# Kernel tuning notes

Hardware: AMD Instinct MI355X
Metric: run time of the kernel (lower is better)

## Reference

```python
import jax, jax.numpy as jnp
import numpy as np

B = 32768
STATE_DIM = 64
ACTION_DIM = 16
HIDDEN = 512
ENSEMBLE = 7
TOP_K = 5
IN_DIM = STATE_DIM + ACTION_DIM          # 80
OUT_DIM = 2 * (STATE_DIM + 1)            # 130 (mu | log_std)


def setup_inputs() -> dict:
    key = jax.random.key(0)
    ks = jax.random.split(key, 12)
    state = jax.random.normal(ks[0], (B, STATE_DIM), dtype=jnp.float32)
    action = jax.random.normal(ks[1], (B, ACTION_DIM), dtype=jnp.float32)
    eps = jax.random.normal(ks[2], (B, STATE_DIM + 1), dtype=jnp.float32)
    # per-sample random expert among the selected subset [0, TOP_K)
    idx = jax.random.randint(ks[3], (B,), 0, TOP_K).astype(jnp.int64)
    # stacked expert params (kaiming-ish scale = 1/sqrt(fan_in))
    W1 = jax.random.normal(ks[4], (ENSEMBLE, IN_DIM, HIDDEN), dtype=jnp.float32) / np.sqrt(IN_DIM)
    b1 = jnp.zeros((ENSEMBLE, HIDDEN), dtype=jnp.float32)
    W2 = jax.random.normal(ks[5], (ENSEMBLE, HIDDEN, HIDDEN), dtype=jnp.float32) / np.sqrt(HIDDEN)
    b2 = jnp.zeros((ENSEMBLE, HIDDEN), dtype=jnp.float32)
    W3 = jax.random.normal(ks[6], (ENSEMBLE, HIDDEN, OUT_DIM), dtype=jnp.float32) / np.sqrt(HIDDEN)
    b3 = jnp.zeros((ENSEMBLE, OUT_DIM), dtype=jnp.float32)
    return {"state": state, "action": action, "eps": eps,
            "W1": W1, "b1": b1, "W2": W2, "b2": b2, "W3": W3, "b3": b3,
            "idx": idx}


def reference(state, action, eps, W1, b1, W2, b2, W3, b3, idx):
    # DynamicsEnsemble.predict: per-sample random expert, Gaussian sample.
    x = jnp.concatenate([state, action], axis=-1)            # [B, IN_DIM]
    # run all experts densely, then gather the routed expert per sample
    h = jax.nn.relu(jnp.einsum('bi,eih->beh', x, W1) + b1)   # [B, E, H]
    h = jax.nn.relu(jnp.einsum('beh,ehk->bek', h, W2) + b2)  # [B, E, H]
    o = jnp.einsum('bek,eko->beo', h, W3) + b3               # [B, E, OUT]
    out = jnp.take_along_axis(o, idx[:, None, None].astype(jnp.int32), axis=1)[:, 0]  # [B, OUT]
    d = state.shape[-1] + 1
    mu = out[:, :d]
    log_std = jnp.clip(out[:, d:], -20.0, 2.0)
    y = mu + jnp.exp(log_std) * eps                          # sampled [delta_state, reward]
    next_state = state + y[:, : state.shape[-1]]
    reward = y[:, state.shape[-1]:]                          # [B, 1]
    return next_state, reward
```

## Files before the change

### kernel.cpp

```cpp
#include <hip/hip_runtime.h>
#include <math.h>

#define B_ROWS     32768
#define STATE_DIM  64
#define ACTION_DIM 16
#define HIDDEN     512
#define ENSEMBLE   7
#define TOP_K      5
#define IN_DIM     80
#define OUT_DIM    130
#define D_OUT      65

#define BM         32
#define MTHREADS   512
#define TILES_PER_E ((B_ROWS + BM - 1) / BM)

#define L1_K8 12
#define L2_K8 64
#define L3_K8 64
#define L3_N  144

#define N_W1 (TOP_K * L1_K8 * HIDDEN * 8)
#define N_W2 (TOP_K * L2_K8 * HIDDEN * 8)
#define N_W3 (TOP_K * L3_K8 * L3_N * 8)

#define OFF_CNT    0
#define OFF_BUCKET 256
#define OFF_W1     (OFF_BUCKET + ENSEMBLE * B_ROWS * 4)
#define OFF_W2     (OFF_W1 + N_W1 * 2)
#define OFF_W3     (OFF_W2 + N_W2 * 2)
#define WS_NEEDED  ((size_t)(OFF_W3 + N_W3 * 2))

#define BUCKET_BLOCKS ((B_ROWS + 255) / 256)
#define PACK_G        (TOP_K * (L1_K8*HIDDEN + L2_K8*HIDDEN + L3_K8*L3_N))
#define PACK_BLOCKS   ((PACK_G + 255) / 256)

typedef __attribute__((ext_vector_type(8))) _Float16 half8;
typedef __attribute__((ext_vector_type(4))) float f32x4;

__global__ void prep_kernel(const int* __restrict__ idx,
                            int* __restrict__ cnt,
                            int* __restrict__ bucket,
                            const float* __restrict__ W1, const float* __restrict__ W2,
                            const float* __restrict__ W3,
                            _Float16* __restrict__ w1, _Float16* __restrict__ w2,
                            _Float16* __restrict__ w3) {
    if (blockIdx.x < BUCKET_BLOCKS) {
        int b = blockIdx.x * 256 + threadIdx.x;
        int lane = threadIdx.x & 63;
        int e = -1;
        if (b < B_ROWS) e = min(max(idx[b], 0), TOP_K - 1);
        #pragma unroll
        for (int ev = 0; ev < TOP_K; ++ev) {
            unsigned long long m = __ballot(e == ev);
            if (m == 0ull) continue;
            int leader = __ffsll((unsigned long long)m) - 1;
            int base = 0;
            if (lane == leader) base = atomicAdd(&cnt[ev], __popcll(m));
            base = __shfl(base, leader);
            if (e == ev) {
                int rank = __popcll(m & ((1ull << lane) - 1ull));
                bucket[ev * B_ROWS + base + rank] = b;
            }
        }
        return;
    }
    const int G1 = L1_K8 * HIDDEN;
    const int G2 = L2_K8 * HIDDEN;
    const int G3 = L3_K8 * L3_N;
    const int GPE = G1 + G2 + G3;
    int g = (blockIdx.x - BUCKET_BLOCKS) * 256 + threadIdx.x;
    if (g >= TOP_K * GPE) return;
    int e = g / GPE, r = g % GPE;

    const float* src; _Float16* dd;
    size_t dst; int k8, n, Kreal, Nreal, srcN;
    if (r < G1) {
        k8 = r / HIDDEN; n = r % HIDDEN;
        src = W1 + (size_t)e * IN_DIM * HIDDEN; Kreal = IN_DIM; Nreal = HIDDEN; srcN = HIDDEN;
        dd = w1; dst = (((size_t)e * L1_K8 + k8) * HIDDEN + n) * 8;
    } else if (r < G1 + G2) {
        int rr = r - G1; k8 = rr / HIDDEN; n = rr % HIDDEN;
        src = W2 + (size_t)e * HIDDEN * HIDDEN; Kreal = HIDDEN; Nreal = HIDDEN; srcN = HIDDEN;
        dd = w2; dst = (((size_t)e * L2_K8 + k8) * HIDDEN + n) * 8;
    } else {
        int rr = r - G1 - G2; k8 = rr / L3_N; n = rr % L3_N;
        src = W3 + (size_t)e * HIDDEN * OUT_DIM; Kreal = HIDDEN; Nreal = OUT_DIM; srcN = OUT_DIM;
        dd = w3; dst = (((size_t)e * L3_K8 + k8) * L3_N + n) * 8;
    }
    half8 hv;
    #pragma unroll
    for (int j = 0; j < 8; ++j) {
        int k = k8 * 8 + j;
        float v = (k < Kreal && n < Nreal) ? src[(size_t)k * srcN + n] : 0.f;
        hv[j] = (_Float16)v;
    }
    *(half8*)(dd + dst) = hv;
}

template<int ASTR, bool SWZ>
__device__ __forceinline__ void gemm_compute(
    const char* A, int ksteps,
    const _Float16* __restrict__ B, int Bn, const float* __restrict__ bias,
    f32x4 (&acc)[2][4], int lane, int col0)
{
    const int lc = lane & 15, kg = lane >> 4;
    #pragma unroll
    for (int ctl = 0; ctl < 4; ++ctl) {
        float b = bias[col0 + ctl * 16 + lc];
        #pragma unroll
        for (int rt = 0; rt < 2; ++rt) acc[rt][ctl] = (f32x4){b, b, b, b};
    }
    const size_t bstep = (size_t)4 * Bn * 8;
    const _Float16* bp = B + ((size_t)kg * Bn + col0 + lc) * 8;

    half8 bc[4], bn[4];
    #pragma unroll
    for (int ctl = 0; ctl < 4; ++ctl) bc[ctl] = *(const half8*)(bp + ctl * 128);

    for (int ks = 0; ks < ksteps; ++ks) {
        if (ks + 1 < ksteps) {
            const _Float16* pn = bp + (size_t)(ks + 1) * bstep;
            #pragma unroll
            for (int ctl = 0; ctl < 4; ++ctl) bn[ctl] = *(const half8*)(pn + ctl * 128);
        }
        half8 ah[2];
        #pragma unroll
        for (int rt = 0; rt < 2; ++rt) {
            int row = rt * 16 + lc;
            int lin = row * ASTR + ks * 64 + kg * 16;
            if (SWZ) lin ^= (row & 7) << 4;
            ah[rt] = *(const half8*)(A + lin);
        }
        #pragma unroll
        for (int rt = 0; rt < 2; ++rt)
        #pragma unroll
        for (int ctl = 0; ctl < 4; ++ctl)
            acc[rt][ctl] = __builtin_amdgcn_mfma_f32_16x16x32_f16(ah[rt], bc[ctl], acc[rt][ctl], 0, 0, 0);
        #pragma unroll
        for (int ctl = 0; ctl < 4; ++ctl) bc[ctl] = bn[ctl];
    }
}

__device__ __forceinline__ void store_h(char* O, f32x4 (&acc)[2][4], int lane, int col0) {
    const int lc = lane & 15, kg = lane >> 4;
    #pragma unroll
    for (int rt = 0; rt < 2; ++rt)
    #pragma unroll
    for (int ctl = 0; ctl < 4; ++ctl)
    #pragma unroll
    for (int q = 0; q < 4; ++q) {
        int row = rt * 16 + kg * 4 + q;
        int col = col0 + ctl * 16 + lc;
        float v = fmaxf(acc[rt][ctl][q], 0.f);
        int lin = (row * 1024 + col * 2) ^ ((row & 7) << 4);
        *(_Float16*)(O + lin) = (_Float16)v;
    }
}

__launch_bounds__(MTHREADS, 4)
__global__ void mlp_mfma_kernel(const float* __restrict__ state,
                                const float* __restrict__ action,
                                const float* __restrict__ eps,
                                const float* __restrict__ b1,
                                const float* __restrict__ b2,
                                const float* __restrict__ b3,
                                const _Float16* __restrict__ w1,
                                const _Float16* __restrict__ w2,
                                const _Float16* __restrict__ w3,
                                const int* __restrict__ cnt, const int* __restrict__ bucket,
                                float* __restrict__ out) {
    __shared__ char smem[39936];
    char* xs = smem;
    char* hs = smem + 7168;
    float* os = (float*)(smem + 7168);

    const int e    = blockIdx.x / TILES_PER_E;
    const int tile = blockIdx.x % TILES_PER_E;
    const int n    = cnt[e];
    const int m0   = tile * BM;
    if (m0 >= n) return;
    const int nrows = min(BM, n - m0);
    const int t = threadIdx.x;
    const int lane = t & 63;
    const int wv = t >> 6;
    const int col0 = wv * 64;
    const int* brow = bucket + (size_t)e * B_ROWS;

    for (int i = t; i < BM * 112; i += MTHREADS) {
        int r = i / 112, c = i % 112;
        int rb = brow[min(m0 + r, n - 1)];
        float v = 0.f;
        if (c < STATE_DIM)      v = state[(size_t)rb * STATE_DIM + c];
        else if (c < IN_DIM)    v = action[(size_t)rb * ACTION_DIM + (c - STATE_DIM)];
        *(_Float16*)(xs + r * 224 + c * 2) = (_Float16)v;
    }
    __syncthreads();

    f32x4 acc[2][4];

    gemm_compute<224, false>(xs, 3,
        w1 + (size_t)e * L1_K8 * HIDDEN * 8,
        HIDDEN, b1 + (size_t)e * HIDDEN, acc, lane, col0);
    store_h(hs, acc, lane, col0);
    __syncthreads();

    gemm_compute<1024, true>(hs, 16,
        w2 + (size_t)e * L2_K8 * HIDDEN * 8,
        HIDDEN, b2 + (size_t)e * HIDDEN, acc, lane, col0);
    __syncthreads();
    store_h(hs, acc, lane, col0);
    __syncthreads();

    {
        const _Float16* Bw = w3 + (size_t)e * L3_K8 * L3_N * 8;
        const float* b3e = b3 + (size_t)e * OUT_DIM;
        const int lc = lane & 15, kg = lane >> 4;
        const int rt  = wv & 1;
        const int ct0 = wv >> 1;
        const bool third = (wv < 2);
        f32x4 o0 = {0.f,0.f,0.f,0.f}, o1 = o0, o2 = o0;
        const size_t bstep = (size_t)4 * L3_N * 8;
        const _Float16* bp0 = Bw + ((size_t)kg * L3_N + ct0 * 16 + lc) * 8;
        const _Float16* bp1 = Bw + ((size_t)kg * L3_N + (ct0 + 4) * 16 + lc) * 8;
        const _Float16* bp2 = Bw + ((size_t)kg * L3_N + 8 * 16 + lc) * 8;
        for (int ks = 0; ks < 16; ++ks) {
            int row = rt * 16 + lc;
            int lin = (row * 1024 + ks * 64 + kg * 16) ^ ((row & 7) << 4);
            half8 ah = *(const half8*)(hs + lin);
            half8 b0 = *(const half8*)(bp0 + (size_t)ks * bstep);
            half8 b1v = *(const half8*)(bp1 + (size_t)ks * bstep);
            o0 = __builtin_amdgcn_mfma_f32_16x16x32_f16(ah, b0, o0, 0, 0, 0);
            o1 = __builtin_amdgcn_mfma_f32_16x16x32_f16(ah, b1v, o1, 0, 0, 0);
            if (third) {
                half8 b2v = *(const half8*)(bp2 + (size_t)ks * bstep);
                o2 = __builtin_amdgcn_mfma_f32_16x16x32_f16(ah, b2v, o2, 0, 0, 0);
            }
        }
        __syncthreads();
        {
            int col = ct0 * 16 + lc;
            #pragma unroll
            for (int q = 0; q < 4; ++q) {
                int row = rt * 16 + kg * 4 + q;
                os[row * 132 + col] = o0[q] + b3e[col];
                if (col + 64 < OUT_DIM) os[row * 132 + col + 64] = o1[q] + b3e[col + 64];
            }
            if (third) {
                int col2 = 128 + lc;
                if (col2 < OUT_DIM) {
                    #pragma unroll
                    for (int q = 0; q < 4; ++q) {
                        int row = rt * 16 + kg * 4 + q;
                        os[row * 132 + col2] = o2[q] + b3e[col2];
                    }
                }
            }
        }
    }
    __syncthreads();

    for (int i = t; i < BM * D_OUT; i += MTHREADS) {
        int r = i / D_OUT, c = i % D_OUT;
        if (r >= nrows) continue;
        int rb = brow[m0 + r];
        float mu = os[r * 132 + c];
        float ls = fminf(fmaxf(os[r * 132 + c + D_OUT], -20.f), 2.f);
        float y  = fmaf(expf(ls), eps[(size_t)rb * D_OUT + c], mu);
        if (c < STATE_DIM) {
            out[(size_t)rb * STATE_DIM + c] = state[(size_t)rb * STATE_DIM + c] + y;
        } else {
            out[(size_t)B_ROWS * STATE_DIM + rb] = y;
        }
    }
}

#define FB_BM      16
#define FB_THREADS 256
#define FB_TILES   ((B_ROWS + FB_BM - 1) / FB_BM)

__launch_bounds__(FB_THREADS, 2)
__global__ void mlp_fp32_kernel(const float* __restrict__ state,
                                const float* __restrict__ action,
                                const float* __restrict__ eps,
                                const float* __restrict__ W1, const float* __restrict__ b1,
                                const float* __restrict__ W2, const float* __restrict__ b2,
                                const float* __restrict__ W3, const float* __restrict__ b3,
                                const int* __restrict__ cnt, const int* __restrict__ bucket,
                                float* __restrict__ out) {
    __shared__ float xs[FB_BM][IN_DIM];
    __shared__ float h1[FB_BM][HIDDEN];
    __shared__ float h2[FB_BM][HIDDEN];
    __shared__ float os[FB_BM][OUT_DIM];
    __shared__ int   rows[FB_BM];

    const int e    = blockIdx.x / FB_TILES;
    const int tile = blockIdx.x % FB_TILES;
    const int n    = cnt[e];
    const int m0   = tile * FB_BM;
    if (m0 >= n) return;
    const int nrows = min(FB_BM, n - m0);
    const int t = threadIdx.x;

    if (t < FB_BM) rows[t] = (t < nrows) ? bucket[e * B_ROWS + m0 + t] : bucket[e * B_ROWS + m0];
    __syncthreads();

    for (int i = t; i < FB_BM * IN_DIM; i += FB_THREADS) {
        int r = i / IN_DIM, c = i % IN_DIM;
        int rb = rows[r];
        xs[r][c] = (c < STATE_DIM) ? state[(size_t)rb * STATE_DIM + c]
                                   : action[(size_t)rb * ACTION_DIM + (c - STATE_DIM)];
    }
    __syncthreads();

    const int c0 = 2 * t;
    {
        const float* We = W1 + (size_t)e * IN_DIM * HIDDEN;
        float acc0[FB_BM], acc1[FB_BM];
        const float bias0 = b1[(size_t)e * HIDDEN + c0];
        const float bias1 = b1[(size_t)e * HIDDEN + c0 + 1];
        #pragma unroll
        for (int r = 0; r < FB_BM; ++r) { acc0[r] = bias0; acc1[r] = bias1; }
        for (int k = 0; k < IN_DIM; k += 4) {
            float2 w0 = *(const float2*)&We[(size_t)(k + 0) * HIDDEN + c0];
            float2 w1v = *(const float2*)&We[(size_t)(k + 1) * HIDDEN + c0];
            float2 w2v = *(const float2*)&We[(size_t)(k + 2) * HIDDEN + c0];
            float2 w3v = *(const float2*)&We[(size_t)(k + 3) * HIDDEN + c0];
            #pragma unroll
            for (int r = 0; r < FB_BM; ++r) {
                float4 x = *(const float4*)&xs[r][k];
                acc0[r] = fmaf(x.x, w0.x, acc0[r]); acc1[r] = fmaf(x.x, w0.y, acc1[r]);
                acc0[r] = fmaf(x.y, w1v.x, acc0[r]); acc1[r] = fmaf(x.y, w1v.y, acc1[r]);
                acc0[r] = fmaf(x.z, w2v.x, acc0[r]); acc1[r] = fmaf(x.z, w2v.y, acc1[r]);
                acc0[r] = fmaf(x.w, w3v.x, acc0[r]); acc1[r] = fmaf(x.w, w3v.y, acc1[r]);
            }
        }
        #pragma unroll
        for (int r = 0; r < FB_BM; ++r)
            *(float2*)&h1[r][c0] = make_float2(fmaxf(acc0[r], 0.f), fmaxf(acc1[r], 0.f));
    }
    __syncthreads();
    {
        const float* We = W2 + (size_t)e * HIDDEN * HIDDEN;
        float acc0[FB_BM], acc1[FB_BM];
        const float bias0 = b2[(size_t)e * HIDDEN + c0];
        const float bias1 = b2[(size_t)e * HIDDEN + c0 + 1];
        #pragma unroll
        for (int r = 0; r < FB_BM; ++r) { acc0[r] = bias0; acc1[r] = bias1; }
        for (int k = 0; k < HIDDEN; k += 4) {
            float2 w0 = *(const float2*)&We[(size_t)(k + 0) * HIDDEN + c0];
            float2 w1v = *(const float2*)&We[(size_t)(k + 1) * HIDDEN + c0];
            float2 w2v = *(const float2*)&We[(size_t)(k + 2) * HIDDEN + c0];
            float2 w3v = *(const float2*)&We[(size_t)(k + 3) * HIDDEN + c0];
            #pragma unroll
            for (int r = 0; r < FB_BM; ++r) {
                float4 x = *(const float4*)&h1[r][k];
                acc0[r] = fmaf(x.x, w0.x, acc0[r]); acc1[r] = fmaf(x.x, w0.y, acc1[r]);
                acc0[r] = fmaf(x.y, w1v.x, acc0[r]); acc1[r] = fmaf(x.y, w1v.y, acc1[r]);
                acc0[r] = fmaf(x.z, w2v.x, acc0[r]); acc1[r] = fmaf(x.z, w2v.y, acc1[r]);
                acc0[r] = fmaf(x.w, w3v.x, acc0[r]); acc1[r] = fmaf(x.w, w3v.y, acc1[r]);
            }
        }
        #pragma unroll
        for (int r = 0; r < FB_BM; ++r)
            *(float2*)&h2[r][c0] = make_float2(fmaxf(acc0[r], 0.f), fmaxf(acc1[r], 0.f));
    }
    __syncthreads();
    {
        const float* We = W3 + (size_t)e * HIDDEN * OUT_DIM;
        for (int i = t; i < FB_BM * OUT_DIM; i += FB_THREADS) {
            int r = i / OUT_DIM, c = i % OUT_DIM;
            float acc = b3[(size_t)e * OUT_DIM + c];
            for (int k = 0; k < HIDDEN; k += 4) {
                float4 h = *(const float4*)&h2[r][k];
                acc = fmaf(h.x, We[(size_t)(k + 0) * OUT_DIM + c], acc);
                acc = fmaf(h.y, We[(size_t)(k + 1) * OUT_DIM + c], acc);
                acc = fmaf(h.z, We[(size_t)(k + 2) * OUT_DIM + c], acc);
                acc = fmaf(h.w, We[(size_t)(k + 3) * OUT_DIM + c], acc);
            }
            os[r][c] = acc;
        }
    }
    __syncthreads();
    for (int i = t; i < FB_BM * D_OUT; i += FB_THREADS) {
        int r = i / D_OUT, c = i % D_OUT;
        if (r >= nrows) continue;
        int rb = rows[r];
        float mu = os[r][c];
        float ls = fminf(fmaxf(os[r][c + D_OUT], -20.f), 2.f);
        float y  = fmaf(expf(ls), eps[(size_t)rb * D_OUT + c], mu);
        if (c < STATE_DIM) out[(size_t)rb * STATE_DIM + c] = state[(size_t)rb * STATE_DIM + c] + y;
        else               out[(size_t)B_ROWS * STATE_DIM + rb] = y;
    }
}

extern "C" void kernel_launch(void* const* d_in, const int* in_sizes, int n_in,
                              void* d_out, int out_size, void* d_ws, size_t ws_size,
                              hipStream_t stream) {
    const float* state  = (const float*)d_in[0];
    const float* action = (const float*)d_in[1];
    const float* eps    = (const float*)d_in[2];
    const float* W1     = (const float*)d_in[3];
    const float* b1     = (const float*)d_in[4];
    const float* W2     = (const float*)d_in[5];
    const float* b2     = (const float*)d_in[6];
    const float* W3     = (const float*)d_in[7];
    const float* b3     = (const float*)d_in[8];
    const int*   idx    = (const int*)d_in[9];
    float* out = (float*)d_out;

    int* cnt    = (int*)((char*)d_ws + OFF_CNT);
    int* bucket = (int*)((char*)d_ws + OFF_BUCKET);

    hipMemsetAsync(cnt, 0, ENSEMBLE * sizeof(int), stream);

    if (ws_size >= WS_NEEDED) {
        _Float16* w1 = (_Float16*)((char*)d_ws + OFF_W1);
        _Float16* w2 = (_Float16*)((char*)d_ws + OFF_W2);
        _Float16* w3 = (_Float16*)((char*)d_ws + OFF_W3);

        prep_kernel<<<BUCKET_BLOCKS + PACK_BLOCKS, 256, 0, stream>>>(
            idx, cnt, bucket, W1, W2, W3, w1, w2, w3);

        mlp_mfma_kernel<<<TOP_K * TILES_PER_E, MTHREADS, 0, stream>>>(
            state, action, eps, b1, b2, b3, w1, w2, w3, cnt, bucket, out);
    } else {
        prep_kernel<<<BUCKET_BLOCKS, 256, 0, stream>>>(
            idx, cnt, bucket, W1, W2, W3, (_Float16*)0, (_Float16*)0, (_Float16*)0);
        mlp_fp32_kernel<<<TOP_K * FB_TILES, FB_THREADS, 0, stream>>>(
            state, action, eps, W1, b1, W2, b2, W3, b3, cnt, bucket, out);
    }
}
```

Baseline: 123.5 us.

## Compact grid to occupied expert tiles with XCD-aware swizzle and unrolled prefetch

```diff
diff --git a/kernel.cpp b/kernel.cpp
--- a/kernel.cpp
+++ b/kernel.cpp
@@ -13,7 +13,7 @@
 
 #define BM         32
 #define MTHREADS   512
-#define TILES_PER_E ((B_ROWS + BM - 1) / BM)
+#define NTILES     (B_ROWS / BM + TOP_K)
 
 #define L1_K8 12
 #define L2_K8 64
@@ -98,9 +98,9 @@
     *(half8*)(dd + dst) = hv;
 }
 
-template<int ASTR, bool SWZ>
+template<int ASTR, bool SWZ, int KSTEPS>
 __device__ __forceinline__ void gemm_compute(
-    const char* A, int ksteps,
+    const char* A,
     const _Float16* __restrict__ B, int Bn, const float* __restrict__ bias,
     f32x4 (&acc)[2][4], int lane, int col0)
 {
@@ -108,21 +108,23 @@
     #pragma unroll
     for (int ctl = 0; ctl < 4; ++ctl) {
         float b = bias[col0 + ctl * 16 + lc];
-        #pragma unroll
-        for (int rt = 0; rt < 2; ++rt) acc[rt][ctl] = (f32x4){b, b, b, b};
+        acc[0][ctl] = (f32x4){b, b, b, b};
+        acc[1][ctl] = acc[0][ctl];
     }
     const size_t bstep = (size_t)4 * Bn * 8;
     const _Float16* bp = B + ((size_t)kg * Bn + col0 + lc) * 8;
 
-    half8 bc[4], bn[4];
-    #pragma unroll
-    for (int ctl = 0; ctl < 4; ++ctl) bc[ctl] = *(const half8*)(bp + ctl * 128);
-
-    for (int ks = 0; ks < ksteps; ++ks) {
-        if (ks + 1 < ksteps) {
+    half8 buf[2][4];
+    #pragma unroll
+    for (int ctl = 0; ctl < 4; ++ctl) buf[0][ctl] = *(const half8*)(bp + ctl * 128);
+
+    #pragma unroll
+    for (int ks = 0; ks < KSTEPS; ++ks) {
+        const int cur = ks & 1, nxt = cur ^ 1;
+        if (ks + 1 < KSTEPS) {
             const _Float16* pn = bp + (size_t)(ks + 1) * bstep;
             #pragma unroll
-            for (int ctl = 0; ctl < 4; ++ctl) bn[ctl] = *(const half8*)(pn + ctl * 128);
+            for (int ctl = 0; ctl < 4; ++ctl) buf[nxt][ctl] = *(const half8*)(pn + ctl * 128);
         }
         half8 ah[2];
         #pragma unroll
@@ -136,9 +138,7 @@
         for (int rt = 0; rt < 2; ++rt)
         #pragma unroll
         for (int ctl = 0; ctl < 4; ++ctl)
-            acc[rt][ctl] = __builtin_amdgcn_mfma_f32_16x16x32_f16(ah[rt], bc[ctl], acc[rt][ctl], 0, 0, 0);
-        #pragma unroll
-        for (int ctl = 0; ctl < 4; ++ctl) bc[ctl] = bn[ctl];
+            acc[rt][ctl] = __builtin_amdgcn_mfma_f32_16x16x32_f16(ah[rt], buf[cur][ctl], acc[rt][ctl], 0, 0, 0);
     }
 }
 
@@ -158,7 +158,14 @@
     }
 }
 
-__launch_bounds__(MTHREADS, 4)
+__device__ __forceinline__ int xcd_swz(int orig) {
+    const int nx = 8, q = NTILES / nx, r = NTILES % nx;
+    int xcd = orig % nx, pos = orig / nx;
+    int base = (xcd < r) ? xcd * (q + 1) : r * (q + 1) + (xcd - r) * q;
+    return base + pos;
+}
+
+__launch_bounds__(MTHREADS, 2)
 __global__ void mlp_mfma_kernel(const float* __restrict__ state,
                                 const float* __restrict__ action,
                                 const float* __restrict__ eps,
@@ -175,9 +182,20 @@
     char* hs = smem + 7168;
     float* os = (float*)(smem + 7168);
 
-    const int e    = blockIdx.x / TILES_PER_E;
-    const int tile = blockIdx.x % TILES_PER_E;
+    const int j = xcd_swz(blockIdx.x);
+    int e = TOP_K, base = 0;
+    {
+        int acct = 0;
+        #pragma unroll
+        for (int ev = 0; ev < TOP_K; ++ev) {
+            int tiles = (cnt[ev] + BM - 1) / BM;
+            if (e == TOP_K && j < acct + tiles) { e = ev; base = acct; }
+            acct += tiles;
+        }
+    }
+    if (e >= TOP_K) return;
     const int n    = cnt[e];
+    const int tile = j - base;
     const int m0   = tile * BM;
     if (m0 >= n) return;
     const int nrows = min(BM, n - m0);
@@ -199,13 +217,13 @@
 
     f32x4 acc[2][4];
 
-    gemm_compute<224, false>(xs, 3,
+    gemm_compute<224, false, 3>(xs,
         w1 + (size_t)e * L1_K8 * HIDDEN * 8,
         HIDDEN, b1 + (size_t)e * HIDDEN, acc, lane, col0);
     store_h(hs, acc, lane, col0);
     __syncthreads();
 
-    gemm_compute<1024, true>(hs, 16,
+    gemm_compute<1024, true, 16>(hs,
         w2 + (size_t)e * L2_K8 * HIDDEN * 8,
         HIDDEN, b2 + (size_t)e * HIDDEN, acc, lane, col0);
     __syncthreads();
@@ -224,18 +242,26 @@
         const _Float16* bp0 = Bw + ((size_t)kg * L3_N + ct0 * 16 + lc) * 8;
         const _Float16* bp1 = Bw + ((size_t)kg * L3_N + (ct0 + 4) * 16 + lc) * 8;
         const _Float16* bp2 = Bw + ((size_t)kg * L3_N + 8 * 16 + lc) * 8;
+
+        half8 p0[2], p1[2], p2[2];
+        p0[0] = *(const half8*)(bp0);
+        p1[0] = *(const half8*)(bp1);
+        if (third) p2[0] = *(const half8*)(bp2);
+
+        #pragma unroll
         for (int ks = 0; ks < 16; ++ks) {
+            const int cur = ks & 1, nxt = cur ^ 1;
+            if (ks + 1 < 16) {
+                p0[nxt] = *(const half8*)(bp0 + (size_t)(ks + 1) * bstep);
+                p1[nxt] = *(const half8*)(bp1 + (size_t)(ks + 1) * bstep);
+                if (third) p2[nxt] = *(const half8*)(bp2 + (size_t)(ks + 1) * bstep);
+            }
             int row = rt * 16 + lc;
             int lin = (row * 1024 + ks * 64 + kg * 16) ^ ((row & 7) << 4);
             half8 ah = *(const half8*)(hs + lin);
-            half8 b0 = *(const half8*)(bp0 + (size_t)ks * bstep);
-            half8 b1v = *(const half8*)(bp1 + (size_t)ks * bstep);
-            o0 = __builtin_amdgcn_mfma_f32_16x16x32_f16(ah, b0, o0, 0, 0, 0);
-            o1 = __builtin_amdgcn_mfma_f32_16x16x32_f16(ah, b1v, o1, 0, 0, 0);
-            if (third) {
-                half8 b2v = *(const half8*)(bp2 + (size_t)ks * bstep);
-                o2 = __builtin_amdgcn_mfma_f32_16x16x32_f16(ah, b2v, o2, 0, 0, 0);
-            }
+            o0 = __builtin_amdgcn_mfma_f32_16x16x32_f16(ah, p0[cur], o0, 0, 0, 0);
+            o1 = __builtin_amdgcn_mfma_f32_16x16x32_f16(ah, p1[cur], o1, 0, 0, 0);
+            if (third) o2 = __builtin_amdgcn_mfma_f32_16x16x32_f16(ah, p2[cur], o2, 0, 0, 0);
         }
         __syncthreads();
         {
@@ -422,7 +448,7 @@
         prep_kernel<<<BUCKET_BLOCKS + PACK_BLOCKS, 256, 0, stream>>>(
             idx, cnt, bucket, W1, W2, W3, w1, w2, w3);
 
-        mlp_mfma_kernel<<<TOP_K * TILES_PER_E, MTHREADS, 0, stream>>>(
+        mlp_mfma_kernel<<<NTILES, MTHREADS, 0, stream>>>(
             state, action, eps, b1, b2, b3, w1, w2, w3, cnt, bucket, out);
     } else {
         prep_kernel<<<BUCKET_BLOCKS, 256, 0, stream>>>(
```

After: 114.3 us. 1.08x faster.
